# Kernel optimization log

Measured on AMD Instinct MI355X. Metric: run time of the kernel, lower is better.

The kernel has to match this reference:

```python
import jax, jax.numpy as jnp
import numpy as np

B, S, H, NH = 2, 2048, 1024, 16
HD = H // NH  # 64
EPS = 1e-5


def setup_inputs() -> dict:
    key = jax.random.key(0)
    ks = jax.random.split(key, 4)
    return {
        "hidden_states": jax.random.normal(ks[0], (B, S, H), dtype=jnp.float32),
        "W_attn": jax.random.normal(ks[1], (H, 3 * H), dtype=jnp.float32) * (1.0 / np.sqrt(H)),
        "b_attn": jnp.zeros((3 * H,), dtype=jnp.float32),
        "W_proj": jax.random.normal(ks[2], (H, H), dtype=jnp.float32) * (1.0 / np.sqrt(H)),
        "b_proj": jnp.zeros((H,), dtype=jnp.float32),
        "q_gamma": jnp.ones((HD,), dtype=jnp.float32),
        "q_beta": jnp.zeros((HD,), dtype=jnp.float32),
        "k_gamma": jnp.ones((HD,), dtype=jnp.float32),
        "k_beta": jnp.zeros((HD,), dtype=jnp.float32),
    }


def _layernorm(x, gamma, beta):
    mu = jnp.mean(x, axis=-1, keepdims=True)
    var = jnp.mean(jnp.square(x - mu), axis=-1, keepdims=True)
    return (x - mu) * jax.lax.rsqrt(var + EPS) * gamma + beta


def reference(hidden_states, W_attn, b_attn, W_proj, b_proj, q_gamma, q_beta, k_gamma, k_beta):
    b, s, h = hidden_states.shape
    qkv = hidden_states @ W_attn + b_attn  # [B,S,3H]
    q, k, v = jnp.split(qkv, 3, axis=-1)
    # [B,S,H] -> [B,NH,S,HD]
    def to_heads(t):
        return t.reshape(b, s, NH, HD).transpose(0, 2, 1, 3)
    q, k, v = to_heads(q), to_heads(k), to_heads(v)
    # QK LayerNorm over head_dim
    q = _layernorm(q, q_gamma, q_beta)
    k = _layernorm(k, k_gamma, k_beta)
    scale = HD ** (-0.5)
    scores = jnp.einsum("bhqd,bhkd->bhqk", q, k) * scale
    causal = jnp.tril(jnp.ones((s, s), dtype=bool))
    mask_value = jnp.finfo(scores.dtype).min
    scores = jnp.where(causal, scores, mask_value)
    attn = jax.nn.softmax(scores.astype(jnp.float32), axis=-1).astype(q.dtype)
    out = jnp.einsum("bhqk,bhkd->bhqd", attn, v)
    out = out.transpose(0, 2, 1, 3).reshape(b, s, h)
    out = out @ W_proj + b_proj
    return out
```

## Files before the change

kernel.cpp:

```cpp
#include <hip/hip_runtime.h>
#include <hip/hip_bf16.h>

typedef __bf16 bf16x8 __attribute__((ext_vector_type(8)));
typedef float f32x4 __attribute__((ext_vector_type(4)));

#define EPS 1e-5f
#define QSCALE 0.18033688011112042f

__device__ __forceinline__ unsigned short f2bf(float f) {
  union { float f; unsigned int i; } c; c.f = f;
  unsigned int r = c.i + 0x7FFFu + ((c.i >> 16) & 1u);
  return (unsigned short)(r >> 16);
}
__device__ __forceinline__ unsigned short f2bf_t(float f) {
  union { float f; unsigned int i; } c; c.f = f;
  return (unsigned short)(c.i >> 16);
}

__device__ __forceinline__ void glds16(const void* g, void* l) {
  __builtin_amdgcn_global_load_lds(
      (const __attribute__((address_space(1))) unsigned int*)g,
      (__attribute__((address_space(3))) unsigned int*)l, 16, 0, 0);
}

__device__ __forceinline__ void transpose_tile(
    const float* __restrict__ in, unsigned short* __restrict__ out,
    int R, int C, int ct0, int rt0, unsigned short* S )
{
  const int t = threadIdx.x;
  const int r = t >> 2, c4 = (t & 3) * 16;
  {
    long base = (long)(rt0 + r) * C + ct0 + c4;
    float4 a = *(const float4*)&in[base];
    float4 b = *(const float4*)&in[base + 4];
    float4 c = *(const float4*)&in[base + 8];
    float4 d = *(const float4*)&in[base + 12];
    unsigned short v[16] = {f2bf(a.x), f2bf(a.y), f2bf(a.z), f2bf(a.w),
                            f2bf(b.x), f2bf(b.y), f2bf(b.z), f2bf(b.w),
                            f2bf(c.x), f2bf(c.y), f2bf(c.z), f2bf(c.w),
                            f2bf(d.x), f2bf(d.y), f2bf(d.z), f2bf(d.w)};
    *(uint4*)&S[r * 72 + c4]     = *(uint4*)&v[0];
    *(uint4*)&S[r * 72 + c4 + 8] = *(uint4*)&v[8];
  }
  __syncthreads();
  unsigned short tmp[16];
#pragma unroll
  for (int j = 0; j < 16; j++) tmp[j] = S[(c4 + j) * 72 + r];
  *(uint4*)&out[(long)(ct0 + r) * R + rt0 + c4]     = *(uint4*)&tmp[0];
  *(uint4*)&out[(long)(ct0 + r) * R + rt0 + c4 + 8] = *(uint4*)&tmp[8];
}

__global__ __launch_bounds__(256) void prep_kernel(
    const float* __restrict__ Wa, const float* __restrict__ Wp,
    const float* __restrict__ X,
    unsigned short* __restrict__ WaT, unsigned short* __restrict__ WpT,
    unsigned short* __restrict__ Xbf)
{
  __shared__ __align__(16) unsigned short S[64 * 72];
  const int id = blockIdx.x;
  if (id < 768) {
    transpose_tile(Wa, WaT, 1024, 3072, (id % 48) * 64, (id / 48) * 64, S);
  } else if (id < 1024) {
    const int i2 = id - 768;
    transpose_tile(Wp, WpT, 1024, 1024, (i2 % 16) * 64, (i2 / 16) * 64, S);
  } else {
    long i = ((long)(id - 1024) * 256 + threadIdx.x) * 16;
    float4 a = *(const float4*)&X[i];
    float4 b = *(const float4*)&X[i + 4];
    float4 c = *(const float4*)&X[i + 8];
    float4 d = *(const float4*)&X[i + 12];
    unsigned short v[16] = {f2bf(a.x), f2bf(a.y), f2bf(a.z), f2bf(a.w),
                            f2bf(b.x), f2bf(b.y), f2bf(b.z), f2bf(b.w),
                            f2bf(c.x), f2bf(c.y), f2bf(c.z), f2bf(c.w),
                            f2bf(d.x), f2bf(d.y), f2bf(d.z), f2bf(d.w)};
    *(uint4*)&Xbf[i]     = *(uint4*)&v[0];
    *(uint4*)&Xbf[i + 8] = *(uint4*)&v[8];
  }
}

__global__ __launch_bounds__(256) void qkvt_kernel(
    const float* __restrict__ Xf,
    const unsigned short* __restrict__ Xbf, int use_xbf,
    const unsigned short* __restrict__ WT,
    const float* __restrict__ bias,
    const float* __restrict__ qg, const float* __restrict__ qb,
    const float* __restrict__ kg, const float* __restrict__ kb,
    unsigned short* __restrict__ Qws, unsigned short* __restrict__ Kws,
    unsigned short* __restrict__ Vt)
{
  __shared__ __align__(16) unsigned short As[2][128 * 32];
  __shared__ __align__(16) unsigned short Bs[2][128 * 32];

  const int tid = threadIdx.x;
  const int w = tid >> 6, lane = tid & 63, quad = lane >> 4, l15 = lane & 15;
  const int mh = w & 1, nh = w >> 1;
  const int id = blockIdx.x;
  const int grow = lane >> 2, gcol = (lane & 3) * 8;

  if (id < 512) {
    const int n0 = (id & 15) * 128, m0 = (id >> 4) * 128;

    f32x4 acc[4][4];
#pragma unroll
    for (int i = 0; i < 4; i++)
#pragma unroll
      for (int j = 0; j < 4; j++) acc[i][j] = (f32x4){0.f, 0.f, 0.f, 0.f};

    if (use_xbf) {
      const long ga = (long)(m0 + w * 32 + grow) * 1024 + gcol;
      const long gb = (long)(n0 + w * 32 + grow) * 1024 + gcol;
#define STAGE_QK(bf, kk) do { \
        glds16(&Xbf[ga + (kk)],             &As[bf][(w * 32) * 32]); \
        glds16(&Xbf[ga + (kk) + 16 * 1024], &As[bf][(w * 32 + 16) * 32]); \
        glds16(&WT[gb + (kk)],              &Bs[bf][(w * 32) * 32]); \
        glds16(&WT[gb + (kk) + 16 * 1024],  &Bs[bf][(w * 32 + 16) * 32]); \
      } while (0)
      STAGE_QK(0, 0);
      __syncthreads();
      int buf = 0;
      for (int kt = 0; kt < 1024; kt += 32) {
        if (kt + 32 < 1024) STAGE_QK(buf ^ 1, kt + 32);
        bf16x8 af[4], bfr[4];
#pragma unroll
        for (int mq = 0; mq < 4; mq++)
          af[mq] = *(const bf16x8*)&As[buf][(mh * 64 + mq * 16 + l15) * 32 + quad * 8];
#pragma unroll
        for (int nq = 0; nq < 4; nq++)
          bfr[nq] = *(const bf16x8*)&Bs[buf][(nh * 64 + nq * 16 + l15) * 32 + quad * 8];
#pragma unroll
        for (int mq = 0; mq < 4; mq++)
#pragma unroll
          for (int nq = 0; nq < 4; nq++)
            acc[mq][nq] = __builtin_amdgcn_mfma_f32_16x16x32_bf16(af[mq], bfr[nq], acc[mq][nq], 0, 0, 0);
        __syncthreads();
        buf ^= 1;
      }
#undef STAGE_QK
    } else {
      const int sr2 = tid >> 1, sh2 = (tid & 1) * 16;
      {
        long xo = (long)(m0 + sr2) * 1024 + sh2;
        float4 a0 = *(const float4*)&Xf[xo];
        float4 a1 = *(const float4*)&Xf[xo + 4];
        float4 a2 = *(const float4*)&Xf[xo + 8];
        float4 a3 = *(const float4*)&Xf[xo + 12];
        unsigned short v[16] = {f2bf(a0.x), f2bf(a0.y), f2bf(a0.z), f2bf(a0.w),
                                f2bf(a1.x), f2bf(a1.y), f2bf(a1.z), f2bf(a1.w),
                                f2bf(a2.x), f2bf(a2.y), f2bf(a2.z), f2bf(a2.w),
                                f2bf(a3.x), f2bf(a3.y), f2bf(a3.z), f2bf(a3.w)};
        *(uint4*)&As[0][sr2 * 32 + sh2]     = *(uint4*)&v[0];
        *(uint4*)&As[0][sr2 * 32 + sh2 + 8] = *(uint4*)&v[8];
        long wo = (long)(n0 + sr2) * 1024 + sh2;
        *(uint4*)&Bs[0][sr2 * 32 + sh2]     = *(const uint4*)&WT[wo];
        *(uint4*)&Bs[0][sr2 * 32 + sh2 + 8] = *(const uint4*)&WT[wo + 8];
      }
      __syncthreads();

      int buf = 0;
      for (int kt = 0; kt < 1024; kt += 32) {
        const int nbuf = buf ^ 1;
        const bool pf = (kt + 32) < 1024;
        uint4 wv0, wv1;
        float4 a0, a1, a2, a3;
        if (pf) {
          long xo = (long)(m0 + sr2) * 1024 + kt + 32 + sh2;
          a0 = *(const float4*)&Xf[xo];
          a1 = *(const float4*)&Xf[xo + 4];
          a2 = *(const float4*)&Xf[xo + 8];
          a3 = *(const float4*)&Xf[xo + 12];
          long wo = (long)(n0 + sr2) * 1024 + kt + 32 + sh2;
          wv0 = *(const uint4*)&WT[wo];
          wv1 = *(const uint4*)&WT[wo + 8];
        }

        bf16x8 af[4], bfr[4];
#pragma unroll
        for (int mq = 0; mq < 4; mq++)
          af[mq] = *(const bf16x8*)&As[buf][(mh * 64 + mq * 16 + l15) * 32 + quad * 8];
#pragma unroll
        for (int nq = 0; nq < 4; nq++)
          bfr[nq] = *(const bf16x8*)&Bs[buf][(nh * 64 + nq * 16 + l15) * 32 + quad * 8];
#pragma unroll
        for (int mq = 0; mq < 4; mq++)
#pragma unroll
          for (int nq = 0; nq < 4; nq++)
            acc[mq][nq] = __builtin_amdgcn_mfma_f32_16x16x32_bf16(af[mq], bfr[nq], acc[mq][nq], 0, 0, 0);

        if (pf) {
          unsigned short v[16] = {f2bf(a0.x), f2bf(a0.y), f2bf(a0.z), f2bf(a0.w),
                                  f2bf(a1.x), f2bf(a1.y), f2bf(a1.z), f2bf(a1.w),
                                  f2bf(a2.x), f2bf(a2.y), f2bf(a2.z), f2bf(a2.w),
                                  f2bf(a3.x), f2bf(a3.y), f2bf(a3.z), f2bf(a3.w)};
          *(uint4*)&As[nbuf][sr2 * 32 + sh2]     = *(uint4*)&v[0];
          *(uint4*)&As[nbuf][sr2 * 32 + sh2 + 8] = *(uint4*)&v[8];
          *(uint4*)&Bs[nbuf][sr2 * 32 + sh2]     = wv0;
          *(uint4*)&Bs[nbuf][sr2 * 32 + sh2 + 8] = wv1;
        }
        __syncthreads();
        buf = nbuf;
      }
    }

#pragma unroll
    for (int nq = 0; nq < 4; nq++) {
      float bv = bias[n0 + nh * 64 + nq * 16 + l15];
#pragma unroll
      for (int mq = 0; mq < 4; mq++)
#pragma unroll
        for (int rr = 0; rr < 4; rr++) acc[mq][nq][rr] += bv;
    }

    const int g = (n0 >> 6) + nh;
    const bool isQ = g < 16;
    {
      float gv[4], bev[4];
#pragma unroll
      for (int nq = 0; nq < 4; nq++) {
        int d = nq * 16 + l15;
        gv[nq]  = isQ ? qg[d] : kg[d];
        bev[nq] = isQ ? qb[d] : kb[d];
        if (isQ) { gv[nq] *= QSCALE; bev[nq] *= QSCALE; }
      }
#pragma unroll
      for (int mq = 0; mq < 4; mq++)
#pragma unroll
        for (int rr = 0; rr < 4; rr++) {
          float s  = acc[mq][0][rr] + acc[mq][1][rr] + acc[mq][2][rr] + acc[mq][3][rr];
          float s2 = acc[mq][0][rr]*acc[mq][0][rr] + acc[mq][1][rr]*acc[mq][1][rr]
                   + acc[mq][2][rr]*acc[mq][2][rr] + acc[mq][3][rr]*acc[mq][3][rr];
#pragma unroll
          for (int off = 1; off < 16; off <<= 1) {
            s  += __shfl_xor(s,  off, 64);
            s2 += __shfl_xor(s2, off, 64);
          }
          float mu   = s * (1.0f / 64.0f);
          float var  = fmaxf(s2 * (1.0f / 64.0f) - mu * mu, 0.f);
          float rstd = rsqrtf(var + EPS);
#pragma unroll
          for (int nq = 0; nq < 4; nq++)
            acc[mq][nq][rr] = (acc[mq][nq][rr] - mu) * rstd * gv[nq] + bev[nq];
        }
    }

    unsigned short* dst = isQ ? Qws : Kws;
    const int head = isQ ? g : g - 16;
#pragma unroll
    for (int mq = 0; mq < 4; mq++)
#pragma unroll
      for (int rr = 0; rr < 4; rr++) {
        int m = m0 + mh * 64 + mq * 16 + quad * 4 + rr;
        int b = m >> 11, s = m & 2047;
        long base = ((long)((b * 16 + head) * 2048 + s)) * 64;
#pragma unroll
        for (int nq = 0; nq < 4; nq++)
          dst[base + nq * 16 + l15] = f2bf(acc[mq][nq][rr]);
      }
  } else {
    const int id2 = id - 512;
    const int n0 = (id2 & 31) * 64, m0 = ((id2 >> 5) & 7) * 128, bz = id2 >> 8;
    const long xrow0 = (long)bz * 2048;
    const unsigned short* WvT = WT + 2048L * 1024;

    f32x4 acc[4][2];
#pragma unroll
    for (int i = 0; i < 4; i++)
#pragma unroll
      for (int j = 0; j < 2; j++) acc[i][j] = (f32x4){0.f, 0.f, 0.f, 0.f};

    if (use_xbf) {
      const long gva = (long)(m0 + w * 32 + grow) * 1024 + gcol;
      const long gvb = (xrow0 + n0 + w * 16 + grow) * 1024 + gcol;
#define STAGE_V(bf, kk) do { \
        glds16(&WvT[gva + (kk)],             &As[bf][(w * 32) * 32]); \
        glds16(&WvT[gva + (kk) + 16 * 1024], &As[bf][(w * 32 + 16) * 32]); \
        glds16(&Xbf[gvb + (kk)],             &Bs[bf][(w * 16) * 32]); \
      } while (0)
      STAGE_V(0, 0);
      __syncthreads();
      int buf = 0;
      for (int kt = 0; kt < 1024; kt += 32) {
        if (kt + 32 < 1024) STAGE_V(buf ^ 1, kt + 32);
        bf16x8 af[4], bfr[2];
#pragma unroll
        for (int mq = 0; mq < 4; mq++)
          af[mq] = *(const bf16x8*)&As[buf][(mh * 64 + mq * 16 + l15) * 32 + quad * 8];
#pragma unroll
        for (int nq = 0; nq < 2; nq++)
          bfr[nq] = *(const bf16x8*)&Bs[buf][(nh * 32 + nq * 16 + l15) * 32 + quad * 8];
#pragma unroll
        for (int mq = 0; mq < 4; mq++)
#pragma unroll
          for (int nq = 0; nq < 2; nq++)
            acc[mq][nq] = __builtin_amdgcn_mfma_f32_16x16x32_bf16(af[mq], bfr[nq], acc[mq][nq], 0, 0, 0);
        __syncthreads();
        buf ^= 1;
      }
#undef STAGE_V
    } else {
      const int srA = tid >> 1, shA = (tid & 1) * 16;
      const int srB = tid >> 2, shB = (tid & 3) * 8;
      {
        long wo = (long)(m0 + srA) * 1024 + shA;
        *(uint4*)&As[0][srA * 32 + shA]     = *(const uint4*)&WvT[wo];
        *(uint4*)&As[0][srA * 32 + shA + 8] = *(const uint4*)&WvT[wo + 8];
        long xo = (xrow0 + n0 + srB) * 1024 + shB;
        float4 a0 = *(const float4*)&Xf[xo];
        float4 a1 = *(const float4*)&Xf[xo + 4];
        unsigned short v[8] = {f2bf(a0.x), f2bf(a0.y), f2bf(a0.z), f2bf(a0.w),
                               f2bf(a1.x), f2bf(a1.y), f2bf(a1.z), f2bf(a1.w)};
        *(uint4*)&Bs[0][srB * 32 + shB] = *(uint4*)v;
      }
      __syncthreads();

      int buf = 0;
      for (int kt = 0; kt < 1024; kt += 32) {
        const int nbuf = buf ^ 1;
        const bool pf = (kt + 32) < 1024;
        uint4 wv0, wv1;
        float4 a0, a1;
        if (pf) {
          long wo = (long)(m0 + srA) * 1024 + kt + 32 + shA;
          wv0 = *(const uint4*)&WvT[wo];
          wv1 = *(const uint4*)&WvT[wo + 8];
          long xo = (xrow0 + n0 + srB) * 1024 + kt + 32 + shB;
          a0 = *(const float4*)&Xf[xo];
          a1 = *(const float4*)&Xf[xo + 4];
        }

        bf16x8 af[4], bfr[2];
#pragma unroll
        for (int mq = 0; mq < 4; mq++)
          af[mq] = *(const bf16x8*)&As[buf][(mh * 64 + mq * 16 + l15) * 32 + quad * 8];
#pragma unroll
        for (int nq = 0; nq < 2; nq++)
          bfr[nq] = *(const bf16x8*)&Bs[buf][(nh * 32 + nq * 16 + l15) * 32 + quad * 8];
#pragma unroll
        for (int mq = 0; mq < 4; mq++)
#pragma unroll
          for (int nq = 0; nq < 2; nq++)
            acc[mq][nq] = __builtin_amdgcn_mfma_f32_16x16x32_bf16(af[mq], bfr[nq], acc[mq][nq], 0, 0, 0);

        if (pf) {
          *(uint4*)&As[nbuf][srA * 32 + shA]     = wv0;
          *(uint4*)&As[nbuf][srA * 32 + shA + 8] = wv1;
          unsigned short v[8] = {f2bf(a0.x), f2bf(a0.y), f2bf(a0.z), f2bf(a0.w),
                                 f2bf(a1.x), f2bf(a1.y), f2bf(a1.z), f2bf(a1.w)};
          *(uint4*)&Bs[nbuf][srB * 32 + shB] = *(uint4*)v;
        }
        __syncthreads();
        buf = nbuf;
      }
    }

    const long outb = (long)bz * 2097152;
#pragma unroll
    for (int mq = 0; mq < 4; mq++)
#pragma unroll
      for (int rr = 0; rr < 4; rr++) {
        int m = m0 + mh * 64 + mq * 16 + quad * 4 + rr;
        float bv = bias[2048 + m];
#pragma unroll
        for (int nq = 0; nq < 2; nq++) {
          int n = n0 + nh * 32 + nq * 16 + l15;
          Vt[outb + (long)m * 2048 + n] = f2bf(acc[mq][nq][rr] + bv);
        }
      }
  }
}

__global__ __launch_bounds__(256) void attn_kernel(
    unsigned short* __restrict__ Qws,
    const unsigned short* __restrict__ Kws,
    const unsigned short* __restrict__ Vt)
{
  __shared__ __align__(16) unsigned short Ks[64 * 72];
  __shared__ __align__(16) unsigned short VTs[64 * 72];
  __shared__ __align__(16) unsigned short Ps[64 * 64];

  const int tid = threadIdx.x;
  const int w = tid >> 6, lane = tid & 63, quad = lane >> 4, l15 = lane & 15;
  const int id = blockIdx.x;
  const int bh = (id & 7) * 4 + ((id >> 3) & 3);
  const int x  = id >> 5;
  const long bhoff = (long)bh * 2048 * 64;
  const long bhv   = (long)bh * 131072;

  const int sr = tid >> 2, sc = (tid & 3) * 16;
  const int qsw = ((sr >> 2) & 3) << 4;
  const int sw = ((l15 >> 2) & 3) << 4;
  const int pc0 = (quad * 8) ^ sw;
  const int pc1 = (32 + quad * 8) ^ sw;

  bf16x8 ones;
  {
    union { unsigned short u[8]; bf16x8 v; } c;
#pragma unroll
    for (int i = 0; i < 8; i++) c.u[i] = 0x3F80u;
    ones = c.v;
  }

#pragma unroll
  for (int ph = 0; ph < 2; ph++) {
    const int qt = ph ? (31 - x) : x;
    const int qbase = qt * 64;
    const int jmax = qt + 1;

    if (ph) __syncthreads();

    *(uint4*)&Ps[sr * 64 + (sc ^ qsw)]       = *(const uint4*)&Qws[bhoff + (qbase + sr) * 64 + sc];
    *(uint4*)&Ps[sr * 64 + ((sc ^ qsw) + 8)] = *(const uint4*)&Qws[bhoff + (qbase + sr) * 64 + sc + 8];
    *(uint4*)&Ks[sr * 72 + sc]      = *(const uint4*)&Kws[bhoff + sr * 64 + sc];
    *(uint4*)&Ks[sr * 72 + sc + 8]  = *(const uint4*)&Kws[bhoff + sr * 64 + sc + 8];
    *(uint4*)&VTs[sr * 72 + sc]     = *(const uint4*)&Vt[bhv + sr * 2048 + sc];
    *(uint4*)&VTs[sr * 72 + sc + 8] = *(const uint4*)&Vt[bhv + sr * 2048 + sc + 8];
    __syncthreads();

    const bf16x8 qf0 = *(const bf16x8*)&Ps[(w * 16 + l15) * 64 + pc0];
    const bf16x8 qf1 = *(const bf16x8*)&Ps[(w * 16 + l15) * 64 + pc1];

    f32x4 o[4], osum;
#pragma unroll
    for (int i = 0; i < 4; i++) o[i] = (f32x4){0.f, 0.f, 0.f, 0.f};
    osum = (f32x4){0.f, 0.f, 0.f, 0.f};

    for (int j = 0; j < jmax; j++) {
      const int kb = j * 64;
      const bool pf = (j + 1) < jmax;
      uint4 pk0, pk1, pv0, pv1;
      if (pf) {
        const int kb1 = kb + 64;
        pk0 = *(const uint4*)&Kws[bhoff + (kb1 + sr) * 64 + sc];
        pk1 = *(const uint4*)&Kws[bhoff + (kb1 + sr) * 64 + sc + 8];
        pv0 = *(const uint4*)&Vt[bhv + sr * 2048 + kb1 + sc];
        pv1 = *(const uint4*)&Vt[bhv + sr * 2048 + kb1 + sc + 8];
      }

      f32x4 sacc[4];
#pragma unroll
      for (int i = 0; i < 4; i++) sacc[i] = (f32x4){0.f, 0.f, 0.f, 0.f};
#pragma unroll
      for (int nt = 0; nt < 4; nt++) {
        bf16x8 kf0 = *(const bf16x8*)&Ks[(nt * 16 + l15) * 72 + quad * 8];
        bf16x8 kf1 = *(const bf16x8*)&Ks[(nt * 16 + l15) * 72 + 32 + quad * 8];
        sacc[nt] = __builtin_amdgcn_mfma_f32_16x16x32_bf16(qf0, kf0, sacc[nt], 0, 0, 0);
        sacc[nt] = __builtin_amdgcn_mfma_f32_16x16x32_bf16(qf1, kf1, sacc[nt], 0, 0, 0);
      }

      const bool domask = (j == qt);
#pragma unroll
      for (int nt = 0; nt < 4; nt++)
#pragma unroll
        for (int rr = 0; rr < 4; rr++) {
          float p = exp2f(sacc[nt][rr]);
          if (domask) {
            int kcol = kb + nt * 16 + l15;
            int qrow = qbase + w * 16 + quad * 4 + rr;
            if (kcol > qrow) p = 0.f;
          }
          sacc[nt][rr] = p;
        }

#pragma unroll
      for (int rr = 0; rr < 4; rr++)
#pragma unroll
        for (int nt = 0; nt < 4; nt++)
          Ps[(w * 16 + quad * 4 + rr) * 64 + (((nt ^ quad) & 3) * 16 + l15)]
              = f2bf_t(sacc[nt][rr]);

      bf16x8 pfr0 = *(const bf16x8*)&Ps[(w * 16 + l15) * 64 + pc0];
      bf16x8 pfr1 = *(const bf16x8*)&Ps[(w * 16 + l15) * 64 + pc1];

      osum = __builtin_amdgcn_mfma_f32_16x16x32_bf16(pfr0, ones, osum, 0, 0, 0);
      osum = __builtin_amdgcn_mfma_f32_16x16x32_bf16(pfr1, ones, osum, 0, 0, 0);
#pragma unroll
      for (int dt = 0; dt < 4; dt++) {
        bf16x8 vf0 = *(const bf16x8*)&VTs[(dt * 16 + l15) * 72 + quad * 8];
        bf16x8 vf1 = *(const bf16x8*)&VTs[(dt * 16 + l15) * 72 + 32 + quad * 8];
        o[dt] = __builtin_amdgcn_mfma_f32_16x16x32_bf16(pfr0, vf0, o[dt], 0, 0, 0);
        o[dt] = __builtin_amdgcn_mfma_f32_16x16x32_bf16(pfr1, vf1, o[dt], 0, 0, 0);
      }

      if (pf) {
        __syncthreads();
        *(uint4*)&Ks[sr * 72 + sc]      = pk0;
        *(uint4*)&Ks[sr * 72 + sc + 8]  = pk1;
        *(uint4*)&VTs[sr * 72 + sc]     = pv0;
        *(uint4*)&VTs[sr * 72 + sc + 8] = pv1;
        __syncthreads();
      }
    }

#pragma unroll
    for (int rr = 0; rr < 4; rr++) {
      float inv = 1.0f / osum[rr];
      int row = qbase + w * 16 + quad * 4 + rr;
      long base = bhoff + (long)row * 64;
#pragma unroll
      for (int dt = 0; dt < 4; dt++)
        Qws[base + dt * 16 + l15] = f2bf(o[dt][rr] * inv);
    }
  }
}

__global__ __launch_bounds__(256) void proj_kernel(
    const unsigned short* __restrict__ AQ,
    const unsigned short* __restrict__ WT,
    const float* __restrict__ bias,
    float* __restrict__ Out)
{
  __shared__ __align__(16) unsigned short As[2][128 * 32];
  __shared__ __align__(16) unsigned short Bs[2][64 * 32];

  const int tid = threadIdx.x;
  const int w = tid >> 6, lane = tid & 63, quad = lane >> 4, l15 = lane & 15;
  const int mh = w & 1, nh = w >> 1;
  const int n0 = blockIdx.x * 64, m0 = blockIdx.y * 128;

  f32x4 acc[4][2];
#pragma unroll
  for (int i = 0; i < 4; i++)
#pragma unroll
    for (int j = 0; j < 2; j++) acc[i][j] = (f32x4){0.f, 0.f, 0.f, 0.f};

  const int grow = lane >> 2, gcolk = (lane & 3) * 8;
  const int m1 = m0 + w * 32 + grow, b1 = m1 >> 11, s1 = m1 & 2047;
  const int m2 = m1 + 16,            b2 = m2 >> 11, s2 = m2 & 2047;
  const long gpb = (long)(n0 + w * 16 + grow) * 1024 + gcolk;

#define STAGE_P(bf, kk) do { \
    int k_ = (kk) + gcolk, h_ = k_ >> 6, d_ = k_ & 63; \
    glds16(&AQ[((long)((b1 * 16 + h_) * 2048 + s1)) * 64 + d_], &As[bf][(w * 32) * 32]); \
    glds16(&AQ[((long)((b2 * 16 + h_) * 2048 + s2)) * 64 + d_], &As[bf][(w * 32 + 16) * 32]); \
    glds16(&WT[gpb + (kk)], &Bs[bf][(w * 16) * 32]); \
  } while (0)

  STAGE_P(0, 0);
  __syncthreads();
  int buf = 0;
  for (int kt = 0; kt < 1024; kt += 32) {
    if (kt + 32 < 1024) STAGE_P(buf ^ 1, kt + 32);
    bf16x8 af[4], bfr[2];
#pragma unroll
    for (int mq = 0; mq < 4; mq++)
      af[mq] = *(const bf16x8*)&As[buf][(mh * 64 + mq * 16 + l15) * 32 + quad * 8];
#pragma unroll
    for (int nq = 0; nq < 2; nq++)
      bfr[nq] = *(const bf16x8*)&Bs[buf][(nh * 32 + nq * 16 + l15) * 32 + quad * 8];
#pragma unroll
    for (int mq = 0; mq < 4; mq++)
#pragma unroll
      for (int nq = 0; nq < 2; nq++)
        acc[mq][nq] = __builtin_amdgcn_mfma_f32_16x16x32_bf16(af[mq], bfr[nq], acc[mq][nq], 0, 0, 0);
    __syncthreads();
    buf ^= 1;
  }
#undef STAGE_P

#pragma unroll
  for (int nq = 0; nq < 2; nq++) {
    int n = n0 + nh * 32 + nq * 16 + l15;
    float bv = bias[n];
#pragma unroll
    for (int mq = 0; mq < 4; mq++)
#pragma unroll
      for (int rr = 0; rr < 4; rr++) {
        int mm = m0 + mh * 64 + mq * 16 + quad * 4 + rr;
        Out[(long)mm * 1024 + n] = acc[mq][nq][rr] + bv;
      }
  }
}

extern "C" void kernel_launch(void* const* d_in, const int* in_sizes, int n_in,
                              void* d_out, int out_size, void* d_ws, size_t ws_size,
                              hipStream_t stream) {
  const float* X  = (const float*)d_in[0];
  const float* Wa = (const float*)d_in[1];
  const float* ba = (const float*)d_in[2];
  const float* Wp = (const float*)d_in[3];
  const float* bp = (const float*)d_in[4];
  const float* qg = (const float*)d_in[5];
  const float* qb = (const float*)d_in[6];
  const float* kg = (const float*)d_in[7];
  const float* kb = (const float*)d_in[8];

  const long per = 2L * 16 * 2048 * 64;
  unsigned short* ws  = (unsigned short*)d_ws;
  unsigned short* Qws = ws;
  unsigned short* Kws = Qws + per;
  unsigned short* Vt  = Kws + per;

  const bool big = ws_size >= (size_t)(5L * per * 2);
  unsigned short *Xbf, *WaT, *WpT;
  if (big) {
    Xbf = Vt + per;
    WaT = Xbf + per;
    WpT = WaT + 3072L * 1024;
  } else {
    Xbf = Qws;
    WaT = Vt + per;
    WpT = WaT + 3072L * 1024;
  }

  prep_kernel<<<big ? 2048 : 1024, 256, 0, stream>>>(Wa, Wp, X, WaT, WpT, Xbf);
  qkvt_kernel<<<1024, 256, 0, stream>>>(X, Xbf, big ? 1 : 0, WaT, ba,
                                        qg, qb, kg, kb, Qws, Kws, Vt);
  attn_kernel<<<512, 256, 0, stream>>>(Qws, Kws, Vt);
  proj_kernel<<<dim3(16, 32), 256, 0, stream>>>(Qws, WpT, bp, (float*)d_out);
}
```

Measured before the change: 214.9 us.

## Triple-buffer GEMM LDS staging, enlarge V tiles, double-buffer attention K/V

The QKV and projection GEMMs move from double- to triple-buffered LDS staging with async global-to-LDS loads. Explicit vmcnt waits plus a raw s_barrier replace __syncthreads, so two tiles stay in flight. The V-transpose GEMM now uses 128x128 tiles instead of 128x64, cutting the grid from 1024 to 768 blocks and reusing each staged tile more. The attention kernel double-buffers K/V in LDS, removing one barrier per iteration. This costs more LDS per block, which can lower occupancy.

```diff
diff --git a/kernel.cpp b/kernel.cpp
--- a/kernel.cpp
+++ b/kernel.cpp
@@ -88,8 +88,8 @@
     unsigned short* __restrict__ Qws, unsigned short* __restrict__ Kws,
     unsigned short* __restrict__ Vt)
 {
-  __shared__ __align__(16) unsigned short As[2][128 * 32];
-  __shared__ __align__(16) unsigned short Bs[2][128 * 32];
+  __shared__ __align__(16) unsigned short As[3][128 * 32];
+  __shared__ __align__(16) unsigned short Bs[3][128 * 32];
 
   const int tid = threadIdx.x;
   const int w = tid >> 6, lane = tid & 63, quad = lane >> 4, l15 = lane & 15;
@@ -97,14 +97,14 @@
   const int id = blockIdx.x;
   const int grow = lane >> 2, gcol = (lane & 3) * 8;
 
+  f32x4 acc[4][4];
+#pragma unroll
+  for (int i = 0; i < 4; i++)
+#pragma unroll
+    for (int j = 0; j < 4; j++) acc[i][j] = (f32x4){0.f, 0.f, 0.f, 0.f};
+
   if (id < 512) {
     const int n0 = (id & 15) * 128, m0 = (id >> 4) * 128;
-
-    f32x4 acc[4][4];
-#pragma unroll
-    for (int i = 0; i < 4; i++)
-#pragma unroll
-      for (int j = 0; j < 4; j++) acc[i][j] = (f32x4){0.f, 0.f, 0.f, 0.f};
 
     if (use_xbf) {
       const long ga = (long)(m0 + w * 32 + grow) * 1024 + gcol;
@@ -116,24 +116,34 @@
         glds16(&WT[gb + (kk) + 16 * 1024],  &Bs[bf][(w * 32 + 16) * 32]); \
       } while (0)
       STAGE_QK(0, 0);
-      __syncthreads();
-      int buf = 0;
+      STAGE_QK(1, 32);
+      asm volatile("s_waitcnt vmcnt(4)" ::: "memory");
+      __builtin_amdgcn_s_barrier();
+      __builtin_amdgcn_sched_barrier(0);
+
+      int cur = 0;
       for (int kt = 0; kt < 1024; kt += 32) {
-        if (kt + 32 < 1024) STAGE_QK(buf ^ 1, kt + 32);
+        int stg = cur + 2; if (stg >= 3) stg -= 3;
+        if (kt + 64 < 1024) STAGE_QK(stg, kt + 64);
         bf16x8 af[4], bfr[4];
 #pragma unroll
         for (int mq = 0; mq < 4; mq++)
-          af[mq] = *(const bf16x8*)&As[buf][(mh * 64 + mq * 16 + l15) * 32 + quad * 8];
+          af[mq] = *(const bf16x8*)&As[cur][(mh * 64 + mq * 16 + l15) * 32 + quad * 8];
 #pragma unroll
         for (int nq = 0; nq < 4; nq++)
-          bfr[nq] = *(const bf16x8*)&Bs[buf][(nh * 64 + nq * 16 + l15) * 32 + quad * 8];
+          bfr[nq] = *(const bf16x8*)&Bs[cur][(nh * 64 + nq * 16 + l15) * 32 + quad * 8];
 #pragma unroll
         for (int mq = 0; mq < 4; mq++)
 #pragma unroll
           for (int nq = 0; nq < 4; nq++)
             acc[mq][nq] = __builtin_amdgcn_mfma_f32_16x16x32_bf16(af[mq], bfr[nq], acc[mq][nq], 0, 0, 0);
-        __syncthreads();
-        buf ^= 1;
+        if (kt + 32 < 1024) {
+          if (kt + 64 < 1024) asm volatile("s_waitcnt vmcnt(4)" ::: "memory");
+          else                asm volatile("s_waitcnt vmcnt(0)" ::: "memory");
+          __builtin_amdgcn_s_barrier();
+          __builtin_amdgcn_sched_barrier(0);
+        }
+        cur = cur + 1; if (cur >= 3) cur -= 3;
       }
 #undef STAGE_QK
     } else {
@@ -257,58 +267,67 @@
       }
   } else {
     const int id2 = id - 512;
-    const int n0 = (id2 & 31) * 64, m0 = ((id2 >> 5) & 7) * 128, bz = id2 >> 8;
+    const int n0 = (id2 & 15) * 128, m0 = ((id2 >> 4) & 7) * 128, bz = id2 >> 7;
     const long xrow0 = (long)bz * 2048;
     const unsigned short* WvT = WT + 2048L * 1024;
 
-    f32x4 acc[4][2];
-#pragma unroll
-    for (int i = 0; i < 4; i++)
-#pragma unroll
-      for (int j = 0; j < 2; j++) acc[i][j] = (f32x4){0.f, 0.f, 0.f, 0.f};
-
     if (use_xbf) {
       const long gva = (long)(m0 + w * 32 + grow) * 1024 + gcol;
-      const long gvb = (xrow0 + n0 + w * 16 + grow) * 1024 + gcol;
+      const long gvb = (xrow0 + n0 + w * 32 + grow) * 1024 + gcol;
 #define STAGE_V(bf, kk) do { \
         glds16(&WvT[gva + (kk)],             &As[bf][(w * 32) * 32]); \
         glds16(&WvT[gva + (kk) + 16 * 1024], &As[bf][(w * 32 + 16) * 32]); \
-        glds16(&Xbf[gvb + (kk)],             &Bs[bf][(w * 16) * 32]); \
+        glds16(&Xbf[gvb + (kk)],             &Bs[bf][(w * 32) * 32]); \
+        glds16(&Xbf[gvb + (kk) + 16 * 1024], &Bs[bf][(w * 32 + 16) * 32]); \
       } while (0)
       STAGE_V(0, 0);
-      __syncthreads();
-      int buf = 0;
+      STAGE_V(1, 32);
+      asm volatile("s_waitcnt vmcnt(4)" ::: "memory");
+      __builtin_amdgcn_s_barrier();
+      __builtin_amdgcn_sched_barrier(0);
+
+      int cur = 0;
       for (int kt = 0; kt < 1024; kt += 32) {
-        if (kt + 32 < 1024) STAGE_V(buf ^ 1, kt + 32);
-        bf16x8 af[4], bfr[2];
-#pragma unroll
-        for (int mq = 0; mq < 4; mq++)
-          af[mq] = *(const bf16x8*)&As[buf][(mh * 64 + mq * 16 + l15) * 32 + quad * 8];
-#pragma unroll
-        for (int nq = 0; nq < 2; nq++)
-          bfr[nq] = *(const bf16x8*)&Bs[buf][(nh * 32 + nq * 16 + l15) * 32 + quad * 8];
-#pragma unroll
-        for (int mq = 0; mq < 4; mq++)
-#pragma unroll
-          for (int nq = 0; nq < 2; nq++)
+        int stg = cur + 2; if (stg >= 3) stg -= 3;
+        if (kt + 64 < 1024) STAGE_V(stg, kt + 64);
+        bf16x8 af[4], bfr[4];
+#pragma unroll
+        for (int mq = 0; mq < 4; mq++)
+          af[mq] = *(const bf16x8*)&As[cur][(mh * 64 + mq * 16 + l15) * 32 + quad * 8];
+#pragma unroll
+        for (int nq = 0; nq < 4; nq++)
+          bfr[nq] = *(const bf16x8*)&Bs[cur][(nh * 64 + nq * 16 + l15) * 32 + quad * 8];
+#pragma unroll
+        for (int mq = 0; mq < 4; mq++)
+#pragma unroll
+          for (int nq = 0; nq < 4; nq++)
             acc[mq][nq] = __builtin_amdgcn_mfma_f32_16x16x32_bf16(af[mq], bfr[nq], acc[mq][nq], 0, 0, 0);
-        __syncthreads();
-        buf ^= 1;
+        if (kt + 32 < 1024) {
+          if (kt + 64 < 1024) asm volatile("s_waitcnt vmcnt(4)" ::: "memory");
+          else                asm volatile("s_waitcnt vmcnt(0)" ::: "memory");
+          __builtin_amdgcn_s_barrier();
+          __builtin_amdgcn_sched_barrier(0);
+        }
+        cur = cur + 1; if (cur >= 3) cur -= 3;
       }
 #undef STAGE_V
     } else {
-      const int srA = tid >> 1, shA = (tid & 1) * 16;
-      const int srB = tid >> 2, shB = (tid & 3) * 8;
+      const int sr2 = tid >> 1, sh2 = (tid & 1) * 16;
       {
-        long wo = (long)(m0 + srA) * 1024 + shA;
-        *(uint4*)&As[0][srA * 32 + shA]     = *(const uint4*)&WvT[wo];
-        *(uint4*)&As[0][srA * 32 + shA + 8] = *(const uint4*)&WvT[wo + 8];
-        long xo = (xrow0 + n0 + srB) * 1024 + shB;
+        long wo = (long)(m0 + sr2) * 1024 + sh2;
+        *(uint4*)&As[0][sr2 * 32 + sh2]     = *(const uint4*)&WvT[wo];
+        *(uint4*)&As[0][sr2 * 32 + sh2 + 8] = *(const uint4*)&WvT[wo + 8];
+        long xo = (xrow0 + n0 + sr2) * 1024 + sh2;
         float4 a0 = *(const float4*)&Xf[xo];
         float4 a1 = *(const float4*)&Xf[xo + 4];
-        unsigned short v[8] = {f2bf(a0.x), f2bf(a0.y), f2bf(a0.z), f2bf(a0.w),
-                               f2bf(a1.x), f2bf(a1.y), f2bf(a1.z), f2bf(a1.w)};
-        *(uint4*)&Bs[0][srB * 32 + shB] = *(uint4*)v;
+        float4 a2 = *(const float4*)&Xf[xo + 8];
+        float4 a3 = *(const float4*)&Xf[xo + 12];
+        unsigned short v[16] = {f2bf(a0.x), f2bf(a0.y), f2bf(a0.z), f2bf(a0.w),
+                                f2bf(a1.x), f2bf(a1.y), f2bf(a1.z), f2bf(a1.w),
+                                f2bf(a2.x), f2bf(a2.y), f2bf(a2.z), f2bf(a2.w),
+                                f2bf(a3.x), f2bf(a3.y), f2bf(a3.z), f2bf(a3.w)};
+        *(uint4*)&Bs[0][sr2 * 32 + sh2]     = *(uint4*)&v[0];
+        *(uint4*)&Bs[0][sr2 * 32 + sh2 + 8] = *(uint4*)&v[8];
       }
       __syncthreads();
 
@@ -317,35 +336,40 @@
         const int nbuf = buf ^ 1;
         const bool pf = (kt + 32) < 1024;
         uint4 wv0, wv1;
-        float4 a0, a1;
+        float4 a0, a1, a2, a3;
         if (pf) {
-          long wo = (long)(m0 + srA) * 1024 + kt + 32 + shA;
+          long wo = (long)(m0 + sr2) * 1024 + kt + 32 + sh2;
           wv0 = *(const uint4*)&WvT[wo];
           wv1 = *(const uint4*)&WvT[wo + 8];
-          long xo = (xrow0 + n0 + srB) * 1024 + kt + 32 + shB;
+          long xo = (xrow0 + n0 + sr2) * 1024 + kt + 32 + sh2;
           a0 = *(const float4*)&Xf[xo];
           a1 = *(const float4*)&Xf[xo + 4];
-        }
-
-        bf16x8 af[4], bfr[2];
+          a2 = *(const float4*)&Xf[xo + 8];
+          a3 = *(const float4*)&Xf[xo + 12];
+        }
+
+        bf16x8 af[4], bfr[4];
 #pragma unroll
         for (int mq = 0; mq < 4; mq++)
           af[mq] = *(const bf16x8*)&As[buf][(mh * 64 + mq * 16 + l15) * 32 + quad * 8];
 #pragma unroll
-        for (int nq = 0; nq < 2; nq++)
-          bfr[nq] = *(const bf16x8*)&Bs[buf][(nh * 32 + nq * 16 + l15) * 32 + quad * 8];
-#pragma unroll
-        for (int mq = 0; mq < 4; mq++)
-#pragma unroll
-          for (int nq = 0; nq < 2; nq++)
+        for (int nq = 0; nq < 4; nq++)
+          bfr[nq] = *(const bf16x8*)&Bs[buf][(nh * 64 + nq * 16 + l15) * 32 + quad * 8];
+#pragma unroll
+        for (int mq = 0; mq < 4; mq++)
+#pragma unroll
+          for (int nq = 0; nq < 4; nq++)
             acc[mq][nq] = __builtin_amdgcn_mfma_f32_16x16x32_bf16(af[mq], bfr[nq], acc[mq][nq], 0, 0, 0);
 
         if (pf) {
-          *(uint4*)&As[nbuf][srA * 32 + shA]     = wv0;
-          *(uint4*)&As[nbuf][srA * 32 + shA + 8] = wv1;
-          unsigned short v[8] = {f2bf(a0.x), f2bf(a0.y), f2bf(a0.z), f2bf(a0.w),
-                                 f2bf(a1.x), f2bf(a1.y), f2bf(a1.z), f2bf(a1.w)};
-          *(uint4*)&Bs[nbuf][srB * 32 + shB] = *(uint4*)v;
+          *(uint4*)&As[nbuf][sr2 * 32 + sh2]     = wv0;
+          *(uint4*)&As[nbuf][sr2 * 32 + sh2 + 8] = wv1;
+          unsigned short v[16] = {f2bf(a0.x), f2bf(a0.y), f2bf(a0.z), f2bf(a0.w),
+                                  f2bf(a1.x), f2bf(a1.y), f2bf(a1.z), f2bf(a1.w),
+                                  f2bf(a2.x), f2bf(a2.y), f2bf(a2.z), f2bf(a2.w),
+                                  f2bf(a3.x), f2bf(a3.y), f2bf(a3.z), f2bf(a3.w)};
+          *(uint4*)&Bs[nbuf][sr2 * 32 + sh2]     = *(uint4*)&v[0];
+          *(uint4*)&Bs[nbuf][sr2 * 32 + sh2 + 8] = *(uint4*)&v[8];
         }
         __syncthreads();
         buf = nbuf;
@@ -360,8 +384,8 @@
         int m = m0 + mh * 64 + mq * 16 + quad * 4 + rr;
         float bv = bias[2048 + m];
 #pragma unroll
-        for (int nq = 0; nq < 2; nq++) {
-          int n = n0 + nh * 32 + nq * 16 + l15;
+        for (int nq = 0; nq < 4; nq++) {
+          int n = n0 + nh * 64 + nq * 16 + l15;
           Vt[outb + (long)m * 2048 + n] = f2bf(acc[mq][nq][rr] + bv);
         }
       }
@@ -373,8 +397,8 @@
     const unsigned short* __restrict__ Kws,
     const unsigned short* __restrict__ Vt)
 {
-  __shared__ __align__(16) unsigned short Ks[64 * 72];
-  __shared__ __align__(16) unsigned short VTs[64 * 72];
+  __shared__ __align__(16) unsigned short Ks[2][64 * 72];
+  __shared__ __align__(16) unsigned short VTs[2][64 * 72];
   __shared__ __align__(16) unsigned short Ps[64 * 64];
 
   const int tid = threadIdx.x;
@@ -409,10 +433,10 @@
 
     *(uint4*)&Ps[sr * 64 + (sc ^ qsw)]       = *(const uint4*)&Qws[bhoff + (qbase + sr) * 64 + sc];
     *(uint4*)&Ps[sr * 64 + ((sc ^ qsw) + 8)] = *(const uint4*)&Qws[bhoff + (qbase + sr) * 64 + sc + 8];
-    *(uint4*)&Ks[sr * 72 + sc]      = *(const uint4*)&Kws[bhoff + sr * 64 + sc];
-    *(uint4*)&Ks[sr * 72 + sc + 8]  = *(const uint4*)&Kws[bhoff + sr * 64 + sc + 8];
-    *(uint4*)&VTs[sr * 72 + sc]     = *(const uint4*)&Vt[bhv + sr * 2048 + sc];
-    *(uint4*)&VTs[sr * 72 + sc + 8] = *(const uint4*)&Vt[bhv + sr * 2048 + sc + 8];
+    *(uint4*)&Ks[0][sr * 72 + sc]      = *(const uint4*)&Kws[bhoff + sr * 64 + sc];
+    *(uint4*)&Ks[0][sr * 72 + sc + 8]  = *(const uint4*)&Kws[bhoff + sr * 64 + sc + 8];
+    *(uint4*)&VTs[0][sr * 72 + sc]     = *(const uint4*)&Vt[bhv + sr * 2048 + sc];
+    *(uint4*)&VTs[0][sr * 72 + sc + 8] = *(const uint4*)&Vt[bhv + sr * 2048 + sc + 8];
     __syncthreads();
 
     const bf16x8 qf0 = *(const bf16x8*)&Ps[(w * 16 + l15) * 64 + pc0];
@@ -423,6 +447,7 @@
     for (int i = 0; i < 4; i++) o[i] = (f32x4){0.f, 0.f, 0.f, 0.f};
     osum = (f32x4){0.f, 0.f, 0.f, 0.f};
 
+    int cb = 0;
     for (int j = 0; j < jmax; j++) {
       const int kb = j * 64;
       const bool pf = (j + 1) < jmax;
@@ -440,8 +465,8 @@
       for (int i = 0; i < 4; i++) sacc[i] = (f32x4){0.f, 0.f, 0.f, 0.f};
 #pragma unroll
       for (int nt = 0; nt < 4; nt++) {
-        bf16x8 kf0 = *(const bf16x8*)&Ks[(nt * 16 + l15) * 72 + quad * 8];
-        bf16x8 kf1 = *(const bf16x8*)&Ks[(nt * 16 + l15) * 72 + 32 + quad * 8];
+        bf16x8 kf0 = *(const bf16x8*)&Ks[cb][(nt * 16 + l15) * 72 + quad * 8];
+        bf16x8 kf1 = *(const bf16x8*)&Ks[cb][(nt * 16 + l15) * 72 + 32 + quad * 8];
         sacc[nt] = __builtin_amdgcn_mfma_f32_16x16x32_bf16(qf0, kf0, sacc[nt], 0, 0, 0);
         sacc[nt] = __builtin_amdgcn_mfma_f32_16x16x32_bf16(qf1, kf1, sacc[nt], 0, 0, 0);
       }
@@ -474,19 +499,20 @@
       osum = __builtin_amdgcn_mfma_f32_16x16x32_bf16(pfr1, ones, osum, 0, 0, 0);
 #pragma unroll
       for (int dt = 0; dt < 4; dt++) {
-        bf16x8 vf0 = *(const bf16x8*)&VTs[(dt * 16 + l15) * 72 + quad * 8];
-        bf16x8 vf1 = *(const bf16x8*)&VTs[(dt * 16 + l15) * 72 + 32 + quad * 8];
+        bf16x8 vf0 = *(const bf16x8*)&VTs[cb][(dt * 16 + l15) * 72 + quad * 8];
+        bf16x8 vf1 = *(const bf16x8*)&VTs[cb][(dt * 16 + l15) * 72 + 32 + quad * 8];
         o[dt] = __builtin_amdgcn_mfma_f32_16x16x32_bf16(pfr0, vf0, o[dt], 0, 0, 0);
         o[dt] = __builtin_amdgcn_mfma_f32_16x16x32_bf16(pfr1, vf1, o[dt], 0, 0, 0);
       }
 
       if (pf) {
+        const int nb = cb ^ 1;
+        *(uint4*)&Ks[nb][sr * 72 + sc]      = pk0;
+        *(uint4*)&Ks[nb][sr * 72 + sc + 8]  = pk1;
+        *(uint4*)&VTs[nb][sr * 72 + sc]     = pv0;
+        *(uint4*)&VTs[nb][sr * 72 + sc + 8] = pv1;
         __syncthreads();
-        *(uint4*)&Ks[sr * 72 + sc]      = pk0;
-        *(uint4*)&Ks[sr * 72 + sc + 8]  = pk1;
-        *(uint4*)&VTs[sr * 72 + sc]     = pv0;
-        *(uint4*)&VTs[sr * 72 + sc + 8] = pv1;
-        __syncthreads();
+        cb = nb;
       }
     }
 
@@ -508,8 +534,8 @@
     const float* __restrict__ bias,
     float* __restrict__ Out)
 {
-  __shared__ __align__(16) unsigned short As[2][128 * 32];
-  __shared__ __align__(16) unsigned short Bs[2][64 * 32];
+  __shared__ __align__(16) unsigned short As[3][128 * 32];
+  __shared__ __align__(16) unsigned short Bs[3][64 * 32];
 
   const int tid = threadIdx.x;
   const int w = tid >> 6, lane = tid & 63, quad = lane >> 4, l15 = lane & 15;
@@ -535,24 +561,34 @@
   } while (0)
 
   STAGE_P(0, 0);
-  __syncthreads();
-  int buf = 0;
+  STAGE_P(1, 32);
+  asm volatile("s_waitcnt vmcnt(3)" ::: "memory");
+  __builtin_amdgcn_s_barrier();
+  __builtin_amdgcn_sched_barrier(0);
+
+  int cur = 0;
   for (int kt = 0; kt < 1024; kt += 32) {
-    if (kt + 32 < 1024) STAGE_P(buf ^ 1, kt + 32);
+    int stg = cur + 2; if (stg >= 3) stg -= 3;
+    if (kt + 64 < 1024) STAGE_P(stg, kt + 64);
     bf16x8 af[4], bfr[2];
 #pragma unroll
     for (int mq = 0; mq < 4; mq++)
-      af[mq] = *(const bf16x8*)&As[buf][(mh * 64 + mq * 16 + l15) * 32 + quad * 8];
+      af[mq] = *(const bf16x8*)&As[cur][(mh * 64 + mq * 16 + l15) * 32 + quad * 8];
 #pragma unroll
     for (int nq = 0; nq < 2; nq++)
-      bfr[nq] = *(const bf16x8*)&Bs[buf][(nh * 32 + nq * 16 + l15) * 32 + quad * 8];
+      bfr[nq] = *(const bf16x8*)&Bs[cur][(nh * 32 + nq * 16 + l15) * 32 + quad * 8];
 #pragma unroll
     for (int mq = 0; mq < 4; mq++)
 #pragma unroll
       for (int nq = 0; nq < 2; nq++)
         acc[mq][nq] = __builtin_amdgcn_mfma_f32_16x16x32_bf16(af[mq], bfr[nq], acc[mq][nq], 0, 0, 0);
-    __syncthreads();
-    buf ^= 1;
+    if (kt + 32 < 1024) {
+      if (kt + 64 < 1024) asm volatile("s_waitcnt vmcnt(3)" ::: "memory");
+      else                asm volatile("s_waitcnt vmcnt(0)" ::: "memory");
+      __builtin_amdgcn_s_barrier();
+      __builtin_amdgcn_sched_barrier(0);
+    }
+    cur = cur + 1; if (cur >= 3) cur -= 3;
   }
 #undef STAGE_P
 
@@ -602,8 +638,8 @@
   }
 
   prep_kernel<<<big ? 2048 : 1024, 256, 0, stream>>>(Wa, Wp, X, WaT, WpT, Xbf);
-  qkvt_kernel<<<1024, 256, 0, stream>>>(X, Xbf, big ? 1 : 0, WaT, ba,
-                                        qg, qb, kg, kb, Qws, Kws, Vt);
+  qkvt_kernel<<<768, 256, 0, stream>>>(X, Xbf, big ? 1 : 0, WaT, ba,
+                                       qg, qb, kg, kb, Qws, Kws, Vt);
   attn_kernel<<<512, 256, 0, stream>>>(Qws, Kws, Vt);
   proj_kernel<<<dim3(16, 32), 256, 0, stream>>>(Qws, WpT, bp, (float*)d_out);
 }
```

Result: no change. 212.7 us (-1.0%).

## Double-buffer attention K/V tiles and use register-staged prefetch in projection GEMM

Applied to the files above, without the earlier changes.

The attention kernel now keeps two LDS buffers for K and V^T tiles, so the next tile is written into the alternate buffer and one of the two barriers per key block is removed. The projection GEMM swaps its global_load_lds direct-to-LDS staging for register-staged loads that are issued before the MFMAs and written to the alternate LDS buffer afterwards. The aim is to cut synchronization stalls and hide global-memory latency behind compute. In exchange, attention LDS use roughly doubles for K/V, which may lower occupancy, and the projection adds register pressure. An unused variable xv0 is also added in the QKV kernel.

```diff
diff --git a/kernel.cpp b/kernel.cpp
--- a/kernel.cpp
+++ b/kernel.cpp
@@ -316,7 +316,7 @@
       for (int kt = 0; kt < 1024; kt += 32) {
         const int nbuf = buf ^ 1;
         const bool pf = (kt + 32) < 1024;
-        uint4 wv0, wv1;
+        uint4 wv0, wv1, xv0;
         float4 a0, a1;
         if (pf) {
           long wo = (long)(m0 + srA) * 1024 + kt + 32 + shA;
@@ -373,8 +373,8 @@
     const unsigned short* __restrict__ Kws,
     const unsigned short* __restrict__ Vt)
 {
-  __shared__ __align__(16) unsigned short Ks[64 * 72];
-  __shared__ __align__(16) unsigned short VTs[64 * 72];
+  __shared__ __align__(16) unsigned short Ks[2][64 * 72];
+  __shared__ __align__(16) unsigned short VTs[2][64 * 72];
   __shared__ __align__(16) unsigned short Ps[64 * 64];
 
   const int tid = threadIdx.x;
@@ -409,10 +409,10 @@
 
     *(uint4*)&Ps[sr * 64 + (sc ^ qsw)]       = *(const uint4*)&Qws[bhoff + (qbase + sr) * 64 + sc];
     *(uint4*)&Ps[sr * 64 + ((sc ^ qsw) + 8)] = *(const uint4*)&Qws[bhoff + (qbase + sr) * 64 + sc + 8];
-    *(uint4*)&Ks[sr * 72 + sc]      = *(const uint4*)&Kws[bhoff + sr * 64 + sc];
-    *(uint4*)&Ks[sr * 72 + sc + 8]  = *(const uint4*)&Kws[bhoff + sr * 64 + sc + 8];
-    *(uint4*)&VTs[sr * 72 + sc]     = *(const uint4*)&Vt[bhv + sr * 2048 + sc];
-    *(uint4*)&VTs[sr * 72 + sc + 8] = *(const uint4*)&Vt[bhv + sr * 2048 + sc + 8];
+    *(uint4*)&Ks[0][sr * 72 + sc]      = *(const uint4*)&Kws[bhoff + sr * 64 + sc];
+    *(uint4*)&Ks[0][sr * 72 + sc + 8]  = *(const uint4*)&Kws[bhoff + sr * 64 + sc + 8];
+    *(uint4*)&VTs[0][sr * 72 + sc]     = *(const uint4*)&Vt[bhv + sr * 2048 + sc];
+    *(uint4*)&VTs[0][sr * 72 + sc + 8] = *(const uint4*)&Vt[bhv + sr * 2048 + sc + 8];
     __syncthreads();
 
     const bf16x8 qf0 = *(const bf16x8*)&Ps[(w * 16 + l15) * 64 + pc0];
@@ -423,6 +423,7 @@
     for (int i = 0; i < 4; i++) o[i] = (f32x4){0.f, 0.f, 0.f, 0.f};
     osum = (f32x4){0.f, 0.f, 0.f, 0.f};
 
+    int cb = 0;
     for (int j = 0; j < jmax; j++) {
       const int kb = j * 64;
       const bool pf = (j + 1) < jmax;
@@ -440,8 +441,8 @@
       for (int i = 0; i < 4; i++) sacc[i] = (f32x4){0.f, 0.f, 0.f, 0.f};
 #pragma unroll
       for (int nt = 0; nt < 4; nt++) {
-        bf16x8 kf0 = *(const bf16x8*)&Ks[(nt * 16 + l15) * 72 + quad * 8];
-        bf16x8 kf1 = *(const bf16x8*)&Ks[(nt * 16 + l15) * 72 + 32 + quad * 8];
+        bf16x8 kf0 = *(const bf16x8*)&Ks[cb][(nt * 16 + l15) * 72 + quad * 8];
+        bf16x8 kf1 = *(const bf16x8*)&Ks[cb][(nt * 16 + l15) * 72 + 32 + quad * 8];
         sacc[nt] = __builtin_amdgcn_mfma_f32_16x16x32_bf16(qf0, kf0, sacc[nt], 0, 0, 0);
         sacc[nt] = __builtin_amdgcn_mfma_f32_16x16x32_bf16(qf1, kf1, sacc[nt], 0, 0, 0);
       }
@@ -474,19 +475,20 @@
       osum = __builtin_amdgcn_mfma_f32_16x16x32_bf16(pfr1, ones, osum, 0, 0, 0);
 #pragma unroll
       for (int dt = 0; dt < 4; dt++) {
-        bf16x8 vf0 = *(const bf16x8*)&VTs[(dt * 16 + l15) * 72 + quad * 8];
-        bf16x8 vf1 = *(const bf16x8*)&VTs[(dt * 16 + l15) * 72 + 32 + quad * 8];
+        bf16x8 vf0 = *(const bf16x8*)&VTs[cb][(dt * 16 + l15) * 72 + quad * 8];
+        bf16x8 vf1 = *(const bf16x8*)&VTs[cb][(dt * 16 + l15) * 72 + 32 + quad * 8];
         o[dt] = __builtin_amdgcn_mfma_f32_16x16x32_bf16(pfr0, vf0, o[dt], 0, 0, 0);
         o[dt] = __builtin_amdgcn_mfma_f32_16x16x32_bf16(pfr1, vf1, o[dt], 0, 0, 0);
       }
 
       if (pf) {
+        const int nb = cb ^ 1;
+        *(uint4*)&Ks[nb][sr * 72 + sc]      = pk0;
+        *(uint4*)&Ks[nb][sr * 72 + sc + 8]  = pk1;
+        *(uint4*)&VTs[nb][sr * 72 + sc]     = pv0;
+        *(uint4*)&VTs[nb][sr * 72 + sc + 8] = pv1;
         __syncthreads();
-        *(uint4*)&Ks[sr * 72 + sc]      = pk0;
-        *(uint4*)&Ks[sr * 72 + sc + 8]  = pk1;
-        *(uint4*)&VTs[sr * 72 + sc]     = pv0;
-        *(uint4*)&VTs[sr * 72 + sc + 8] = pv1;
-        __syncthreads();
+        cb = nb;
       }
     }
 
@@ -522,23 +524,34 @@
 #pragma unroll
     for (int j = 0; j < 2; j++) acc[i][j] = (f32x4){0.f, 0.f, 0.f, 0.f};
 
-  const int grow = lane >> 2, gcolk = (lane & 3) * 8;
-  const int m1 = m0 + w * 32 + grow, b1 = m1 >> 11, s1 = m1 & 2047;
-  const int m2 = m1 + 16,            b2 = m2 >> 11, s2 = m2 & 2047;
-  const long gpb = (long)(n0 + w * 16 + grow) * 1024 + gcolk;
-
-#define STAGE_P(bf, kk) do { \
-    int k_ = (kk) + gcolk, h_ = k_ >> 6, d_ = k_ & 63; \
-    glds16(&AQ[((long)((b1 * 16 + h_) * 2048 + s1)) * 64 + d_], &As[bf][(w * 32) * 32]); \
-    glds16(&AQ[((long)((b2 * 16 + h_) * 2048 + s2)) * 64 + d_], &As[bf][(w * 32 + 16) * 32]); \
-    glds16(&WT[gpb + (kk)], &Bs[bf][(w * 16) * 32]); \
-  } while (0)
-
-  STAGE_P(0, 0);
+  const int srA = tid >> 1, shA = (tid & 1) * 16;
+  const int srB = tid >> 2, shB = (tid & 3) * 8;
+  const int m = m0 + srA, b = m >> 11, s = m & 2047;
+
+  {
+    const int h = shA >> 6, d = shA & 63;
+    long ao = ((long)((b * 16 + h) * 2048 + s)) * 64 + d;
+    *(uint4*)&As[0][srA * 32 + shA]     = *(const uint4*)&AQ[ao];
+    *(uint4*)&As[0][srA * 32 + shA + 8] = *(const uint4*)&AQ[ao + 8];
+    long wo = (long)(n0 + srB) * 1024 + shB;
+    *(uint4*)&Bs[0][srB * 32 + shB] = *(const uint4*)&WT[wo];
+  }
   __syncthreads();
+
   int buf = 0;
   for (int kt = 0; kt < 1024; kt += 32) {
-    if (kt + 32 < 1024) STAGE_P(buf ^ 1, kt + 32);
+    const int nbuf = buf ^ 1;
+    const bool pf = (kt + 32) < 1024;
+    uint4 av0, av1, wv0;
+    if (pf) {
+      const int k = kt + 32 + shA, h = k >> 6, d = k & 63;
+      long ao = ((long)((b * 16 + h) * 2048 + s)) * 64 + d;
+      av0 = *(const uint4*)&AQ[ao];
+      av1 = *(const uint4*)&AQ[ao + 8];
+      long wo = (long)(n0 + srB) * 1024 + kt + 32 + shB;
+      wv0 = *(const uint4*)&WT[wo];
+    }
+
     bf16x8 af[4], bfr[2];
 #pragma unroll
     for (int mq = 0; mq < 4; mq++)
@@ -551,10 +564,15 @@
 #pragma unroll
       for (int nq = 0; nq < 2; nq++)
         acc[mq][nq] = __builtin_amdgcn_mfma_f32_16x16x32_bf16(af[mq], bfr[nq], acc[mq][nq], 0, 0, 0);
+
+    if (pf) {
+      *(uint4*)&As[nbuf][srA * 32 + shA]     = av0;
+      *(uint4*)&As[nbuf][srA * 32 + shA + 8] = av1;
+      *(uint4*)&Bs[nbuf][srB * 32 + shB]     = wv0;
+    }
     __syncthreads();
-    buf ^= 1;
-  }
-#undef STAGE_P
+    buf = nbuf;
+  }
 
 #pragma unroll
   for (int nq = 0; nq < 2; nq++) {
```

Measured after the change: 207.9 us. 3.3% less time.
